# Kernel tuning notes

Hardware: AMD Instinct MI355X
Metric: run time of the kernel (lower is better)

The kernel has to match this reference:

```python
import jax, jax.numpy as jnp
import numpy as np

B, S, D, H, AD, E = 4, 2048, 1024, 2048, 128, 8

def _ln(x, g, b, eps=1e-5):
    m = jnp.mean(x, axis=-1, keepdims=True)
    v = jnp.var(x, axis=-1, keepdims=True)
    return (x - m) * jax.lax.rsqrt(v + eps) * g + b

def setup_inputs() -> dict:
    key = jax.random.key(0)
    ks = jax.random.split(key, 12)
    scale = 1.0 / D ** 0.5
    ascale = scale * 0.01
    ead = 0.01 / AD ** 0.5
    return {
        'x': jax.random.normal(ks[0], (B, S, D), jnp.float32),
        'expert_weights': jax.random.uniform(ks[1], (B, S, E), jnp.float32),
        'Wu': jax.random.normal(ks[2], (H, D), jnp.float32) * scale,
        'bu': jnp.zeros((H,), jnp.float32),
        'Wg': jax.random.normal(ks[3], (H, D), jnp.float32) * scale,
        'bg': jnp.zeros((H,), jnp.float32),
        'Wd': jax.random.normal(ks[4], (D, H), jnp.float32) * scale,
        'bd': jnp.zeros((D,), jnp.float32),
        'Wpre': jax.random.normal(ks[5], (AD, D), jnp.float32) * ascale,
        'bpre': jnp.zeros((AD,), jnp.float32),
        'Wpost': jax.random.normal(ks[6], (AD, H), jnp.float32) * ascale,
        'bpost': jnp.zeros((AD,), jnp.float32),
        'ln_g': jnp.ones((AD,), jnp.float32),
        'ln_b': jnp.zeros((AD,), jnp.float32),
        'Wap': jax.random.normal(ks[7], (H, AD), jnp.float32) * ascale,
        'A': jax.random.normal(ks[8], (E, AD, AD), jnp.float32) * ead,
        'eg': jnp.ones((E, AD), jnp.float32),
        'eb': jnp.zeros((E, AD), jnp.float32),
        'Wp': jax.random.normal(ks[9], (H, AD), jnp.float32) * ead,
        'Wo': jax.random.normal(ks[10], (D, H), jnp.float32) * ead,
    }

def reference(x, expert_weights, Wu, bu, Wg, bg, Wd, bd, Wpre, bpre, Wpost, bpost, ln_g, ln_b, Wap, A, eg, eb, Wp, Wo):
    # ---- SharedExpertMLP ----
    up = x @ Wu.T + bu                      # [B,S,H]
    gate = x @ Wg.T + bg
    hidden = jax.nn.silu(gate) * up
    adapt_in = _ln(x @ Wpre.T + bpre, ln_g, ln_b)        # [B,S,AD]
    adapt_out = _ln(hidden @ Wpost.T + bpost, ln_g, ln_b)
    aw = jnp.einsum('bsa,bta->bst', adapt_in, adapt_out)  # [B,S,S]
    aw = jax.nn.silu(jnp.clip(aw, -5.0, 5.0))
    adapt = jnp.einsum('bst,bta->bsa', aw, adapt_in)
    hidden = hidden + 0.1 * (adapt @ Wap.T)
    shared = hidden @ Wd.T + bd                           # [B,S,D]
    # ---- expert branch (vectorized over experts) ----
    pre = x @ Wpre.T + bpre                               # [B,S,AD] (no adapt_norm here, as in torch)
    h = jnp.einsum('bsa,eca->ebsc', pre, A)               # per-expert adapter linear
    h = _ln(h, eg[:, None, None, :], eb[:, None, None, :])
    wmask = jnp.where(expert_weights > 0, expert_weights, 0.0)  # [B,S,E]
    hw = jnp.einsum('ebsa,bse->bsa', h, wmask)            # weighted combine before shared projections
    Wc = Wo @ Wp                                          # [D,AD]: output_proj(expert_proj(.))
    contrib = hw @ Wc.T                                   # [B,S,D]
    # sum_i w_i * (shared + 0.1*mask_i*expert_i) = shared*sum(w) + 0.1*sum(w_i*expert_i)
    return shared * jnp.sum(expert_weights, axis=-1, keepdims=True) + 0.1 * contrib
```

## Files before the change

kernel.cpp:

```cpp
#include <hip/hip_runtime.h>
#include <math.h>

#define BB 4
#define SS 2048
#define DD 1024
#define HH 2048
#define AD 128
#define EE 8
#define MM (BB*SS)
#define PS 136

typedef unsigned short u16;
typedef short bf16x8 __attribute__((ext_vector_type(8)));
typedef float f32x4 __attribute__((ext_vector_type(4)));
typedef float f32x16 __attribute__((ext_vector_type(16)));

__device__ __forceinline__ float silu_f(float x){ return x / (1.f + __expf(-x)); }

__device__ __forceinline__ u16 f2bf(float f){
    union { float f; unsigned u; } c; c.f = f;
    unsigned r = (c.u + 0x7FFFu + ((c.u >> 16) & 1u)) >> 16;
    return (u16)r;
}

__device__ __forceinline__ void gld16(const u16* g, u16* l){
    __builtin_amdgcn_global_load_lds((const __attribute__((address_space(1))) void*)g,
                                     (__attribute__((address_space(3))) void*)l, 16, 0, 0);
}

#define VMCNT(n) asm volatile("s_waitcnt vmcnt(" #n ")" ::: "memory")

__global__ __launch_bounds__(256,2) void mfma_sk(
    const u16* __restrict__ A, const u16* __restrict__ B, float* __restrict__ P,
    int M, int K, int S, long sA, long sB, long sC, long sSplit)
{
    __shared__ __align__(16) u16 As[128*32];
    __shared__ __align__(16) u16 Bs[128*32];
    const int t = threadIdx.x;
    const int lane = t & 63;
    const int wv = t >> 6;
    const int s = blockIdx.x;
    const int m0 = blockIdx.y * 128;
    const u16* Ab = A + (long)blockIdx.z * sA;
    const u16* Bb = B + (long)blockIdx.z * sB;
    const int srow = t >> 2, scol = (t & 3) * 8;
    const int Ks = K / S, kBeg = s * Ks;
    const u16* ga0 = Ab + (long)(m0 + srow) * K + scol + kBeg;
    const u16* ga1 = ga0 + 64L * K;
    const u16* gb0 = Bb + (long)srow * K + scol + kBeg;
    const u16* gb1 = gb0 + 64L * K;
    u16* la0 = As + t * 8;  u16* la1 = As + 2048 + t * 8;
    u16* lb0 = Bs + t * 8;  u16* lb1 = Bs + 2048 + t * 8;
    const int fr = lane & 15, q = lane >> 4;
    const int wm = (wv & 1) * 64, wn = (wv >> 1) * 64;

    f32x4 acc[4][4] = {};
    for (int k0 = 0; k0 < Ks; k0 += 32) {
        gld16(ga0 + k0, la0);
        gld16(ga1 + k0, la1);
        gld16(gb0 + k0, lb0);
        gld16(gb1 + k0, lb1);
        __syncthreads();
        bf16x8 af[4], bfr[4];
        #pragma unroll
        for (int i = 0; i < 4; ++i) af[i]  = *(const bf16x8*)&As[(wm + i*16 + fr)*32 + q*8];
        #pragma unroll
        for (int i = 0; i < 4; ++i) bfr[i] = *(const bf16x8*)&Bs[(wn + i*16 + fr)*32 + q*8];
        #pragma unroll
        for (int mi = 0; mi < 4; ++mi)
            #pragma unroll
            for (int ni = 0; ni < 4; ++ni)
                acc[mi][ni] = __builtin_amdgcn_mfma_f32_16x16x32_bf16(af[mi], bfr[ni], acc[mi][ni], 0, 0, 0);
        __syncthreads();
    }

    float* Pf = P + (long)s * sSplit + (long)blockIdx.z * sC;
    #pragma unroll
    for (int mi = 0; mi < 4; ++mi)
        #pragma unroll
        for (int ni = 0; ni < 4; ++ni) {
            const int col = wn + ni*16 + fr;
            #pragma unroll
            for (int r = 0; r < 4; ++r) {
                const int row = m0 + wm + mi*16 + q*4 + r;
                Pf[(long)row * 128 + col] = acc[mi][ni][r];
            }
        }
}

__global__ __launch_bounds__(256,2) void mfma_upgate(
    const u16* __restrict__ X, const u16* __restrict__ Wu_, const u16* __restrict__ Wg_,
    const float* __restrict__ bu, const float* __restrict__ bg, u16* __restrict__ H)
{
    __shared__ __align__(16) u16 lds[36864];
    const int t = threadIdx.x, lane = t & 63, wv = t >> 6;
    const int l31 = lane & 31, kh = lane >> 5;
    const int wr = wv & 1, wc = wv >> 1;
    const int m0 = blockIdx.y * 128, n0 = blockIdx.x * 128;

    const int srow = t >> 2;
    const int gcol = (((t & 3) ^ ((t >> 3) & 3)) * 8);
    const u16* gx = X   + (long)(m0 + srow) * DD + gcol;
    const u16* gu = Wu_ + (long)(n0 + srow) * DD + gcol;
    const u16* gg = Wg_ + (long)(n0 + srow) * DD + gcol;
    const int st8 = t * 8;

    const int sw3 = (l31 >> 1) & 3;
    int offA[2][2], offU[2][2], offG[2][2];
    #pragma unroll
    for (int m = 0; m < 2; ++m)
        #pragma unroll
        for (int ks = 0; ks < 2; ++ks) {
            const int ko = ((ks*2 + kh) ^ sw3) * 8;
            offA[m][ks] =        (wr*64 + m*32 + l31)*32 + ko;
            offU[m][ks] = 4096 + (wc*64 + m*32 + l31)*32 + ko;
            offG[m][ks] = 8192 + (wc*64 + m*32 + l31)*32 + ko;
        }

    f32x16 accU[2][2] = {};
    f32x16 accG[2][2] = {};

    auto stage = [&](int tb) {
        u16* Lb = lds + (tb % 3) * 12288;
        const int k0 = tb * 32;
        gld16(gx + k0,           Lb + st8);
        gld16(gx + 64L*DD + k0,  Lb + 2048 + st8);
        gld16(gu + k0,           Lb + 4096 + st8);
        gld16(gu + 64L*DD + k0,  Lb + 6144 + st8);
        gld16(gg + k0,           Lb + 8192 + st8);
        gld16(gg + 64L*DD + k0,  Lb + 10240 + st8);
    };

    auto compute = [&](int tb) {
        const u16* Lb = lds + (tb % 3) * 12288;
        bf16x8 a[2][2], uf[2][2], gf[2][2];
        #pragma unroll
        for (int n = 0; n < 2; ++n)
            #pragma unroll
            for (int ks = 0; ks < 2; ++ks) {
                uf[n][ks] = *(const bf16x8*)&Lb[offU[n][ks]];
                gf[n][ks] = *(const bf16x8*)&Lb[offG[n][ks]];
            }
        #pragma unroll
        for (int m = 0; m < 2; ++m)
            #pragma unroll
            for (int ks = 0; ks < 2; ++ks)
                a[m][ks] = *(const bf16x8*)&Lb[offA[m][ks]];
        __builtin_amdgcn_s_setprio(1);
        #pragma unroll
        for (int m = 0; m < 2; ++m)
            #pragma unroll
            for (int n = 0; n < 2; ++n)
                #pragma unroll
                for (int ks = 0; ks < 2; ++ks) {
                    accU[m][n] = __builtin_amdgcn_mfma_f32_32x32x16_bf16(a[m][ks], uf[n][ks], accU[m][n], 0, 0, 0);
                    accG[m][n] = __builtin_amdgcn_mfma_f32_32x32x16_bf16(a[m][ks], gf[n][ks], accG[m][n], 0, 0, 0);
                }
        __builtin_amdgcn_s_setprio(0);
    };

    stage(0); stage(1);
    #pragma unroll 1
    for (int tt = 0; tt < 30; ++tt) {
        VMCNT(6);
        __builtin_amdgcn_s_barrier();
        __builtin_amdgcn_sched_barrier(0);
        stage(tt + 2);
        compute(tt);
    }
    VMCNT(6);
    __builtin_amdgcn_s_barrier();
    __builtin_amdgcn_sched_barrier(0);
    compute(30);
    VMCNT(0);
    __builtin_amdgcn_s_barrier();
    __builtin_amdgcn_sched_barrier(0);
    compute(31);

    #pragma unroll
    for (int n = 0; n < 2; ++n) {
        const int col = n0 + wc*64 + n*32 + l31;
        const float bub = bu[col], bgb = bg[col];
        #pragma unroll
        for (int m = 0; m < 2; ++m)
            #pragma unroll
            for (int r = 0; r < 16; ++r) {
                const int row = m0 + wr*64 + m*32 + (r & 3) + 8*(r >> 2) + 4*kh;
                const float u = accU[m][n][r] + bub;
                const float g = accG[m][n][r] + bgb;
                H[(long)row * HH + col] = f2bf(silu_f(g) * u);
            }
    }
}

__global__ __launch_bounds__(256,2) void mfma_final(
    const u16* __restrict__ Hh, const u16* __restrict__ Wd_,
    const u16* __restrict__ Ac, const u16* __restrict__ Wcat,
    const float* __restrict__ bd, const float* __restrict__ sumw,
    float* __restrict__ out)
{
    __shared__ __align__(16) u16 lds[24576];
    const int t = threadIdx.x, lane = t & 63, wv = t >> 6;
    const int l31 = lane & 31, kh = lane >> 5;
    const int wr = wv & 1, wc = wv >> 1;
    const int m0 = blockIdx.y * 128, n0 = blockIdx.x * 128;

    const int srow = t >> 2;
    const int gcol = (((t & 3) ^ ((t >> 3) & 3)) * 8);
    const u16* gA1 = Hh   + (long)(m0 + srow) * HH  + gcol;
    const u16* gB1 = Wd_  + (long)(n0 + srow) * HH  + gcol;
    const u16* gA2 = Ac   + (long)(m0 + srow) * 256 + gcol;
    const u16* gB2 = Wcat + (long)(n0 + srow) * 256 + gcol;
    const int st8 = t * 8;

    const int sw3 = (l31 >> 1) & 3;
    int offA[2][2], offB[2][2];
    #pragma unroll
    for (int m = 0; m < 2; ++m)
        #pragma unroll
        for (int ks = 0; ks < 2; ++ks) {
            const int ko = ((ks*2 + kh) ^ sw3) * 8;
            offA[m][ks] =        (wr*64 + m*32 + l31)*32 + ko;
            offB[m][ks] = 4096 + (wc*64 + m*32 + l31)*32 + ko;
        }

    f32x16 acc[2][2]  = {};
    f32x16 acc2[2][2] = {};

    auto stage = [&](int tk) {
        u16* Lb = lds + (tk % 3) * 8192;
        if (tk < 64) {
            const int k0 = tk * 32;
            gld16(gA1 + k0,           Lb + st8);
            gld16(gA1 + 64L*HH + k0,  Lb + 2048 + st8);
            gld16(gB1 + k0,           Lb + 4096 + st8);
            gld16(gB1 + 64L*HH + k0,  Lb + 6144 + st8);
        } else {
            const int k0 = (tk - 64) * 32;
            gld16(gA2 + k0,           Lb + st8);
            gld16(gA2 + 64L*256 + k0, Lb + 2048 + st8);
            gld16(gB2 + k0,           Lb + 4096 + st8);
            gld16(gB2 + 64L*256 + k0, Lb + 6144 + st8);
        }
    };

    auto compute = [&](int tk, f32x16 (&A)[2][2]) {
        const u16* Lb = lds + (tk % 3) * 8192;
        bf16x8 a[2][2], b[2][2];
        #pragma unroll
        for (int m = 0; m < 2; ++m)
            #pragma unroll
            for (int ks = 0; ks < 2; ++ks) {
                a[m][ks] = *(const bf16x8*)&Lb[offA[m][ks]];
                b[m][ks] = *(const bf16x8*)&Lb[offB[m][ks]];
            }
        __builtin_amdgcn_s_setprio(1);
        #pragma unroll
        for (int m = 0; m < 2; ++m)
            #pragma unroll
            for (int n = 0; n < 2; ++n)
                #pragma unroll
                for (int ks = 0; ks < 2; ++ks)
                    A[m][n] = __builtin_amdgcn_mfma_f32_32x32x16_bf16(a[m][ks], b[n][ks], A[m][n], 0, 0, 0);
        __builtin_amdgcn_s_setprio(0);
    };

    stage(0); stage(1);
    #pragma unroll 1
    for (int tt = 0; tt < 70; ++tt) {
        VMCNT(4);
        __builtin_amdgcn_s_barrier();
        __builtin_amdgcn_sched_barrier(0);
        stage(tt + 2);
        if (tt < 64) compute(tt, acc); else compute(tt, acc2);
    }
    VMCNT(4);
    __builtin_amdgcn_s_barrier();
    __builtin_amdgcn_sched_barrier(0);
    compute(70, acc2);
    VMCNT(0);
    __builtin_amdgcn_s_barrier();
    __builtin_amdgcn_sched_barrier(0);
    compute(71, acc2);

    #pragma unroll
    for (int n = 0; n < 2; ++n) {
        const int col = n0 + wc*64 + n*32 + l31;
        const float bdc = bd[col];
        #pragma unroll
        for (int m = 0; m < 2; ++m)
            #pragma unroll
            for (int r = 0; r < 16; ++r) {
                const int row = m0 + wr*64 + m*32 + (r & 3) + 8*(r >> 2) + 4*kh;
                out[(long)row * DD + col] =
                    sumw[row] * (acc[m][n][r] + bdc) + 0.1f * acc2[m][n][r];
            }
    }
}

__global__ __launch_bounds__(256,2) void flash_pv(
    const u16* __restrict__ ai, const u16* __restrict__ ao,
    const u16* __restrict__ aiT, float* __restrict__ adaptP)
{
    __shared__ __align__(16) u16 As[128*32];
    __shared__ __align__(16) u16 Bs[128*32];
    __shared__ __align__(16) u16 Psh[128*PS];
    const int t = threadIdx.x, lane = t & 63, wv = t >> 6;
    const int fr = lane & 15, q = lane >> 4;
    const int wm = (wv & 1) * 64, wn = (wv >> 1) * 64;
    const int tg = blockIdx.x, s0 = blockIdx.y * 128, b = blockIdx.z;
    const u16* aib  = ai  + (long)b * SS * AD;
    const u16* aob  = ao  + (long)b * SS * AD;
    const u16* aiTb = aiT + (long)b * AD * SS;
    const int srow = t >> 2, scol = (t & 3) * 8;
    u16* la0 = As + t * 8;  u16* la1 = As + 2048 + t * 8;
    u16* lb0 = Bs + t * 8;  u16* lb1 = Bs + 2048 + t * 8;
    const u16* ga0 = aib + (long)(s0 + srow) * AD + scol;
    const u16* ga1 = ga0 + 64L * AD;

    f32x4 vacc[4][4] = {};
    for (int ti = 0; ti < 2; ++ti) {
        const int t0 = tg * 256 + ti * 128;
        const u16* gb0 = aob + (long)(t0 + srow) * AD + scol;
        const u16* gb1 = gb0 + 64L * AD;
        f32x4 acc[4][4] = {};
        for (int k0 = 0; k0 < AD; k0 += 32) {
            gld16(ga0 + k0, la0);
            gld16(ga1 + k0, la1);
            gld16(gb0 + k0, lb0);
            gld16(gb1 + k0, lb1);
            __syncthreads();
            bf16x8 af[4], bfr[4];
            #pragma unroll
            for (int i = 0; i < 4; ++i) af[i]  = *(const bf16x8*)&As[(wm + i*16 + fr)*32 + q*8];
            #pragma unroll
            for (int i = 0; i < 4; ++i) bfr[i] = *(const bf16x8*)&Bs[(wn + i*16 + fr)*32 + q*8];
            #pragma unroll
            for (int mi = 0; mi < 4; ++mi)
                #pragma unroll
                for (int ni = 0; ni < 4; ++ni)
                    acc[mi][ni] = __builtin_amdgcn_mfma_f32_16x16x32_bf16(af[mi], bfr[ni], acc[mi][ni], 0, 0, 0);
            __syncthreads();
        }
        #pragma unroll
        for (int mi = 0; mi < 4; ++mi)
            #pragma unroll
            for (int ni = 0; ni < 4; ++ni)
                #pragma unroll
                for (int r = 0; r < 4; ++r) {
                    float v = acc[mi][ni][r];
                    v = fminf(fmaxf(v, -5.f), 5.f);
                    Psh[(wm + mi*16 + q*4 + r)*PS + wn + ni*16 + fr] = f2bf(silu_f(v));
                }
        __syncthreads();
        #pragma unroll
        for (int kk = 0; kk < 4; ++kk) {
            bf16x8 pf[4], bi[4];
            #pragma unroll
            for (int mi = 0; mi < 4; ++mi)
                pf[mi] = *(const bf16x8*)&Psh[(wm + mi*16 + fr)*PS + kk*32 + q*8];
            #pragma unroll
            for (int ni = 0; ni < 4; ++ni)
                bi[ni] = *(const bf16x8*)&aiTb[(long)(wn + ni*16 + fr)*SS + t0 + kk*32 + q*8];
            #pragma unroll
            for (int mi = 0; mi < 4; ++mi)
                #pragma unroll
                for (int ni = 0; ni < 4; ++ni)
                    vacc[mi][ni] = __builtin_amdgcn_mfma_f32_16x16x32_bf16(pf[mi], bi[ni], vacc[mi][ni], 0, 0, 0);
        }
    }
    float* Pf = adaptP + (long)tg * MM * AD + (long)(b * SS + s0) * AD;
    #pragma unroll
    for (int mi = 0; mi < 4; ++mi)
        #pragma unroll
        for (int ni = 0; ni < 4; ++ni) {
            const int col = wn + ni*16 + fr;
            #pragma unroll
            for (int r = 0; r < 4; ++r) {
                const int row = wm + mi*16 + q*4 + r;
                Pf[(long)row * AD + col] = vacc[mi][ni][r];
            }
        }
}

__global__ __launch_bounds__(256) void scale_adapt(
    const float* __restrict__ P, const float* __restrict__ sumw, u16* __restrict__ acat)
{
    const int i = blockIdx.x * 256 + threadIdx.x;
    float4 v = ((const float4*)P)[i];
    #pragma unroll
    for (int tg = 1; tg < 8; ++tg) {
        const float4 w = ((const float4*)P)[i + (long)tg * (MM*AD/4)];
        v.x += w.x; v.y += w.y; v.z += w.z; v.w += w.w;
    }
    const long grow = i >> 5;
    const float sw = sumw[grow];
    ushort4 o;
    o.x = f2bf(sw*v.x); o.y = f2bf(sw*v.y); o.z = f2bf(sw*v.z); o.w = f2bf(sw*v.w);
    ((ushort4*)acat)[grow*64 + 32 + (i & 31)] = o;
}

__global__ __launch_bounds__(256) void expert_fused(
    const u16* __restrict__ pre, const u16* __restrict__ aexp,
    const float* __restrict__ ew, const float* __restrict__ eg,
    const float* __restrict__ eb, u16* __restrict__ acat,
    float* __restrict__ sumw)
{
    __shared__ float ewsh[32*8];
    __shared__ float egsh[8*128], ebsh[8*128];
    __shared__ float part[32*132];
    const int t = threadIdx.x, lane = t & 63, wv = t >> 6;
    const int fr = lane & 15, q = lane >> 4;
    const int wm = (wv & 1) * 16;
    const int e0 = (wv >> 1) * 4;
    const int m0 = blockIdx.x * 32;
    if (t < 64) {
        const int row = t >> 1, j = (t & 1)*4;
        *(float4*)&ewsh[row*8+j] = *(const float4*)&ew[(long)(m0+row)*EE + j];
    }
    {   const int e = t >> 5, c = (t & 31)*4;
        *(float4*)&egsh[e*128+c] = *(const float4*)&eg[e*128+c];
        *(float4*)&ebsh[e*128+c] = *(const float4*)&eb[e*128+c]; }
    __syncthreads();

    f32x4 hwacc[8] = {};
    for (int ee = 0; ee < 4; ++ee) {
        const int e = e0 + ee;
        f32x4 acc[8] = {};
        const u16* Ae = aexp + (long)e * AD * AD;
        #pragma unroll
        for (int ks = 0; ks < 4; ++ks) {
            bf16x8 af, bfr[8];
            af = *(const bf16x8*)&pre[(long)(m0 + wm + fr)*AD + ks*32 + q*8];
            #pragma unroll
            for (int ni = 0; ni < 8; ++ni)
                bfr[ni] = *(const bf16x8*)&Ae[(long)(ni*16 + fr)*AD + ks*32 + q*8];
            #pragma unroll
            for (int ni = 0; ni < 8; ++ni)
                acc[ni] = __builtin_amdgcn_mfma_f32_16x16x32_bf16(af, bfr[ni], acc[ni], 0, 0, 0);
        }
        #pragma unroll
        for (int r = 0; r < 4; ++r) {
            float s = 0.f, s2 = 0.f;
            #pragma unroll
            for (int ni = 0; ni < 8; ++ni) { const float v = acc[ni][r]; s += v; s2 += v*v; }
            #pragma unroll
            for (int msk = 1; msk < 16; msk <<= 1) {
                s  += __shfl_xor(s,  msk, 64);
                s2 += __shfl_xor(s2, msk, 64);
            }
            const float mean = s * (1.f/128.f);
            const float var  = s2 * (1.f/128.f) - mean*mean;
            const float rs   = rsqrtf(var + 1e-5f);
            const int rowl = wm + q*4 + r;
            float w = ewsh[rowl*8 + e]; w = w > 0.f ? w : 0.f;
            #pragma unroll
            for (int ni = 0; ni < 8; ++ni) {
                const int col = ni*16 + fr;
                hwacc[ni][r] += w * ((acc[ni][r] - mean) * rs * egsh[e*128+col] + ebsh[e*128+col]);
            }
        }
    }
    if (wv >= 2) {
        #pragma unroll
        for (int r = 0; r < 4; ++r) {
            const int rowl = wm + q*4 + r;
            #pragma unroll
            for (int ni = 0; ni < 8; ++ni)
                part[rowl*132 + ni*16 + fr] = hwacc[ni][r];
        }
    }
    __syncthreads();
    if (wv < 2) {
        #pragma unroll
        for (int r = 0; r < 4; ++r) {
            const int rowl = wm + q*4 + r;
            #pragma unroll
            for (int ni = 0; ni < 8; ++ni) {
                const float v = hwacc[ni][r] + part[rowl*132 + ni*16 + fr];
                acat[(long)(m0+rowl)*256 + ni*16 + fr] = f2bf(v);
            }
            if (fr == 0) {
                float sw = 0.f;
                #pragma unroll
                for (int j = 0; j < 8; ++j) sw += ewsh[rowl*8 + j];
                sumw[m0 + rowl] = sw;
            }
        }
    }
}

template<int S>
__global__ __launch_bounds__(128) void ln_reduce(
    const float* __restrict__ P, long sSplit, const float* __restrict__ bias,
    u16* __restrict__ raw, u16* __restrict__ ln_out,
    const float* __restrict__ g, const float* __restrict__ b)
{
    const int r = blockIdx.x, tid = threadIdx.x;
    float v = bias[tid];
    #pragma unroll
    for (int s = 0; s < S; ++s) v += P[(long)s * sSplit + (long)r * AD + tid];
    if (raw) raw[(long)r * AD + tid] = f2bf(v);
    __shared__ float red[AD], red2[AD];
    red[tid] = v; red2[tid] = v*v;
    __syncthreads();
    for (int s = 64; s > 0; s >>= 1) {
        if (tid < s) { red[tid] += red[tid+s]; red2[tid] += red2[tid+s]; }
        __syncthreads();
    }
    const float mean = red[0] * (1.f/AD);
    const float var  = red2[0] * (1.f/AD) - mean*mean;
    const float rs   = rsqrtf(var + 1e-5f);
    ln_out[(long)r * AD + tid] = f2bf((v - mean) * rs * g[tid] + b[tid]);
}

__global__ __launch_bounds__(256) void reduce_cat(
    const float* __restrict__ P, u16* __restrict__ Wcat)
{
    const int i = blockIdx.x * 256 + threadIdx.x;
    const int a4 = i & 31, z = (i >> 5) & 1, d = i >> 6;
    const float* src = P + (long)z * (16L*DD*AD) + (long)d * AD + a4*4;
    float4 v = *(const float4*)src;
    #pragma unroll
    for (int s = 1; s < 16; ++s) {
        const float4 w = *(const float4*)(src + (long)s * DD * AD);
        v.x += w.x; v.y += w.y; v.z += w.z; v.w += w.w;
    }
    ushort4 o; o.x=f2bf(v.x); o.y=f2bf(v.y); o.z=f2bf(v.z); o.w=f2bf(v.w);
    ((ushort4*)Wcat)[(long)d*64 + z*32 + a4] = o;
}

__global__ __launch_bounds__(256) void transpose6(
    const u16* __restrict__ wRaw, u16* __restrict__ wT,
    const u16* __restrict__ ai, u16* __restrict__ aiT)
{
    __shared__ u16 tile[32][33];
    const int z = blockIdx.z;
    const u16* in; u16* out;
    if (z < 2) { in = wRaw + (long)z * HH * AD; out = wT + (long)z * AD * HH; }
    else       { in = ai + (long)(z-2) * SS * AD; out = aiT + (long)(z-2) * AD * SS; }
    const int x0 = blockIdx.x * 32, y0 = blockIdx.y * 32;
    const int tx = threadIdx.x & 31, ty = threadIdx.x >> 5;
    #pragma unroll
    for (int j = 0; j < 4; ++j)
        tile[ty + j*8][tx] = in[(long)(y0 + ty + j*8) * AD + x0 + tx];
    __syncthreads();
    #pragma unroll
    for (int j = 0; j < 4; ++j)
        out[(long)(x0 + ty + j*8) * SS + y0 + tx] = tile[tx][ty + j*8];
}

struct Cvt5 { const float* in[5]; u16* out[5]; long cum[6]; };
__global__ __launch_bounds__(256) void cvt_pack(Cvt5 a)
{
    const long i = (long)blockIdx.x * 256 + threadIdx.x;
    if (i >= a.cum[5]) return;
    int s = 0;
    while (i >= a.cum[s+1]) ++s;
    const long j = i - a.cum[s];
    const float4 v = ((const float4*)a.in[s])[j];
    ushort4 o;
    o.x = f2bf(v.x); o.y = f2bf(v.y); o.z = f2bf(v.z); o.w = f2bf(v.w);
    ((ushort4*)a.out[s])[j] = o;
}

extern "C" void kernel_launch(void* const* d_in, const int* in_sizes, int n_in,
                              void* d_out, int out_size, void* d_ws, size_t ws_size,
                              hipStream_t stream) {
    const float* x    = (const float*)d_in[0];
    const float* ew   = (const float*)d_in[1];
    const float* Wu   = (const float*)d_in[2];
    const float* bu   = (const float*)d_in[3];
    const float* Wg   = (const float*)d_in[4];
    const float* bg   = (const float*)d_in[5];
    const float* Wd   = (const float*)d_in[6];
    const float* bd   = (const float*)d_in[7];
    const float* Wpre = (const float*)d_in[8];
    const float* bpre = (const float*)d_in[9];
    const float* Wpost= (const float*)d_in[10];
    const float* bpost= (const float*)d_in[11];
    const float* ln_g = (const float*)d_in[12];
    const float* ln_b = (const float*)d_in[13];
    const float* Wap  = (const float*)d_in[14];
    const float* Aex  = (const float*)d_in[15];
    const float* eg   = (const float*)d_in[16];
    const float* eb   = (const float*)d_in[17];
    const float* Wp   = (const float*)d_in[18];
    const float* Wo   = (const float*)d_in[19];
    float* out = (float*)d_out;

    char* p = (char*)d_ws;
    auto take = [&](long bytes) -> char* {
        char* r = p; p += (bytes + 255) & ~255L; return r;
    };
    u16* x_slot  = (u16*)take(16777216);
    u16* wslot   = (u16*)take((long)2*DD*HH*2);
    u16* wpre    = (u16*)take((long)AD*DD*2);
    u16* aex     = (u16*)take((long)EE*AD*AD*2);
    u16* pre_bf  = (u16*)take((long)MM*AD*2);
    u16* ai_bf   = (u16*)take((long)MM*AD*2);
    char* shareA = take(33554432);
    u16* acat    = (u16*)take((long)MM*256*2);
    float* sumw  = (float*)take((long)MM*4);
    u16* hidden  = (u16*)take((long)MM*HH*2);

    u16* x_bf    = x_slot;
    u16* aiT     = x_slot;
    u16* wRaw    = aiT  + 1048576;
    u16* wT      = wRaw + 524288;
    u16* wpost_w = wT   + 524288;
    u16* wcat    = wpost_w + 262144;
    u16* ao_bf   = wcat + 262144;
    float* preP   = (float*)shareA;
    float* wcP    = (float*)(shareA + 16777216);
    float* wpostP = (float*)shareA;
    float* adaptP = (float*)shareA;

    {
        Cvt5 a;
        a.in[0]=x;    a.out[0]=x_bf;              long n0=(long)MM*DD/4;
        a.in[1]=Wu;   a.out[1]=wslot;             long n1=(long)HH*DD/4;
        a.in[2]=Wg;   a.out[2]=wslot+(long)DD*HH; long n2=(long)HH*DD/4;
        a.in[3]=Wpre; a.out[3]=wpre;              long n3=(long)AD*DD/4;
        a.in[4]=Aex;  a.out[4]=aex;               long n4=(long)EE*AD*AD/4;
        a.cum[0]=0; a.cum[1]=n0; a.cum[2]=n0+n1; a.cum[3]=n0+n1+n2;
        a.cum[4]=n0+n1+n2+n3; a.cum[5]=n0+n1+n2+n3+n4;
        cvt_pack<<<dim3((a.cum[5]+255)/256), 256, 0, stream>>>(a);
    }
    mfma_sk<<<dim3(4, MM/128, 1), 256, 0, stream>>>(
        x_bf, wpre, preP, MM, DD, 4, 0, 0, 0, (long)MM*AD);
    ln_reduce<4><<<dim3(MM), 128, 0, stream>>>(preP, (long)MM*AD, bpre, pre_bf, ai_bf, ln_g, ln_b);
    expert_fused<<<dim3(MM/32), 256, 0, stream>>>(pre_bf, aex, ew, eg, eb, acat, sumw);
    mfma_upgate<<<dim3(HH/128, MM/128), 256, 0, stream>>>(
        x_bf, wslot, wslot+(long)DD*HH, bu, bg, hidden);
    {
        Cvt5 a;
        a.in[0]=Wo;    a.out[0]=wslot;             long n0=(long)DD*HH/4;
        a.in[1]=Wd;    a.out[1]=wslot+(long)DD*HH; long n1=(long)DD*HH/4;
        a.in[2]=Wpost; a.out[2]=wpost_w;           long n2=(long)AD*HH/4;
        a.in[3]=Wp;    a.out[3]=wRaw;              long n3=(long)HH*AD/4;
        a.in[4]=Wap;   a.out[4]=wRaw+(long)HH*AD;  long n4=(long)HH*AD/4;
        a.cum[0]=0; a.cum[1]=n0; a.cum[2]=n0+n1; a.cum[3]=n0+n1+n2;
        a.cum[4]=n0+n1+n2+n3; a.cum[5]=n0+n1+n2+n3+n4;
        cvt_pack<<<dim3((a.cum[5]+255)/256), 256, 0, stream>>>(a);
    }
    transpose6<<<dim3(4,64,6), 256, 0, stream>>>(wRaw, wT, ai_bf, aiT);
    mfma_sk<<<dim3(16, DD/128, 2), 256, 0, stream>>>(
        wslot, wT, wcP, DD, HH, 16, (long)DD*HH, (long)AD*HH, 16L*DD*AD, (long)DD*AD);
    reduce_cat<<<dim3(256), 256, 0, stream>>>(wcP, wcat);
    mfma_sk<<<dim3(8, MM/128, 1), 256, 0, stream>>>(
        hidden, wpost_w, wpostP, MM, HH, 8, 0, 0, 0, (long)MM*AD);
    ln_reduce<8><<<dim3(MM), 128, 0, stream>>>(wpostP, (long)MM*AD, bpost, nullptr, ao_bf, ln_g, ln_b);
    flash_pv<<<dim3(8, SS/128, BB), 256, 0, stream>>>(ai_bf, ao_bf, aiT, adaptP);
    scale_adapt<<<dim3((long)MM*AD/4/256), 256, 0, stream>>>(adaptP, sumw, acat);
    mfma_final<<<dim3(DD/128, MM/128), 256, 0, stream>>>(
        hidden, wslot+(long)DD*HH, acat, wcat, bd, sumw, out);
}
```

Before: 398.4 us.

## Enlarge upgate GEMM tile to 256x128 with 512 threads and 4-stage pipeline

Restructures the fused up/gate GEMM kernel to use 512-thread blocks, each covering 256 rows by 128 columns. Each wave now computes a 128x32 tile, and the LDS pipeline deepens from 3 to 4 stages using 128KB of shared memory. The larger tile is meant to cut redundant weight loads from global memory per output and to hide more load latency. The cost is higher LDS usage, which may limit occupancy to one block per CU, plus a changed register footprint per thread.

```diff
diff --git a/kernel.cpp b/kernel.cpp
--- a/kernel.cpp
+++ b/kernel.cpp
@@ -88,87 +88,86 @@
         }
 }
 
-__global__ __launch_bounds__(256,2) void mfma_upgate(
+__global__ __launch_bounds__(512,2) void mfma_upgate(
     const u16* __restrict__ X, const u16* __restrict__ Wu_, const u16* __restrict__ Wg_,
     const float* __restrict__ bu, const float* __restrict__ bg, u16* __restrict__ H)
 {
-    __shared__ __align__(16) u16 lds[36864];
+    __shared__ __align__(16) u16 lds[65536];
     const int t = threadIdx.x, lane = t & 63, wv = t >> 6;
     const int l31 = lane & 31, kh = lane >> 5;
-    const int wr = wv & 1, wc = wv >> 1;
-    const int m0 = blockIdx.y * 128, n0 = blockIdx.x * 128;
+    const int wr = wv >> 2, wc = wv & 3;
+    const int m0 = blockIdx.y * 256, n0 = blockIdx.x * 128;
 
     const int srow = t >> 2;
     const int gcol = (((t & 3) ^ ((t >> 3) & 3)) * 8);
-    const u16* gx = X   + (long)(m0 + srow) * DD + gcol;
-    const u16* gu = Wu_ + (long)(n0 + srow) * DD + gcol;
-    const u16* gg = Wg_ + (long)(n0 + srow) * DD + gcol;
+    const u16* gx0 = X   + (long)(m0 + srow) * DD + gcol;
+    const u16* gx1 = gx0 + 128L * DD;
+    const u16* gu  = Wu_ + (long)(n0 + srow) * DD + gcol;
+    const u16* gg  = Wg_ + (long)(n0 + srow) * DD + gcol;
     const int st8 = t * 8;
 
     const int sw3 = (l31 >> 1) & 3;
-    int offA[2][2], offU[2][2], offG[2][2];
-    #pragma unroll
-    for (int m = 0; m < 2; ++m)
+    int offA[4][2], offB[2];
+    #pragma unroll
+    for (int m = 0; m < 4; ++m)
+        #pragma unroll
+        for (int ks = 0; ks < 2; ++ks)
+            offA[m][ks] = (wr*128 + m*32 + l31)*32 + (((ks*2 + kh) ^ sw3) * 8);
+    #pragma unroll
+    for (int ks = 0; ks < 2; ++ks)
+        offB[ks] = (wc*32 + l31)*32 + (((ks*2 + kh) ^ sw3) * 8);
+
+    f32x16 accU[4] = {};
+    f32x16 accG[4] = {};
+
+    auto stage = [&](int tb) {
+        u16* Lb = lds + (tb & 3) * 16384;
+        const int k0 = tb * 32;
+        gld16(gx0 + k0, Lb + st8);
+        gld16(gx1 + k0, Lb + 4096 + st8);
+        gld16(gu  + k0, Lb + 8192 + st8);
+        gld16(gg  + k0, Lb + 12288 + st8);
+    };
+
+    auto compute = [&](int tb) {
+        const u16* Lb = lds + (tb & 3) * 16384;
+        bf16x8 a[4][2], uf[2], gf[2];
         #pragma unroll
         for (int ks = 0; ks < 2; ++ks) {
-            const int ko = ((ks*2 + kh) ^ sw3) * 8;
-            offA[m][ks] =        (wr*64 + m*32 + l31)*32 + ko;
-            offU[m][ks] = 4096 + (wc*64 + m*32 + l31)*32 + ko;
-            offG[m][ks] = 8192 + (wc*64 + m*32 + l31)*32 + ko;
-        }
-
-    f32x16 accU[2][2] = {};
-    f32x16 accG[2][2] = {};
-
-    auto stage = [&](int tb) {
-        u16* Lb = lds + (tb % 3) * 12288;
-        const int k0 = tb * 32;
-        gld16(gx + k0,           Lb + st8);
-        gld16(gx + 64L*DD + k0,  Lb + 2048 + st8);
-        gld16(gu + k0,           Lb + 4096 + st8);
-        gld16(gu + 64L*DD + k0,  Lb + 6144 + st8);
-        gld16(gg + k0,           Lb + 8192 + st8);
-        gld16(gg + 64L*DD + k0,  Lb + 10240 + st8);
-    };
-
-    auto compute = [&](int tb) {
-        const u16* Lb = lds + (tb % 3) * 12288;
-        bf16x8 a[2][2], uf[2][2], gf[2][2];
-        #pragma unroll
-        for (int n = 0; n < 2; ++n)
-            #pragma unroll
-            for (int ks = 0; ks < 2; ++ks) {
-                uf[n][ks] = *(const bf16x8*)&Lb[offU[n][ks]];
-                gf[n][ks] = *(const bf16x8*)&Lb[offG[n][ks]];
-            }
-        #pragma unroll
-        for (int m = 0; m < 2; ++m)
+            uf[ks] = *(const bf16x8*)&Lb[8192  + offB[ks]];
+            gf[ks] = *(const bf16x8*)&Lb[12288 + offB[ks]];
+        }
+        #pragma unroll
+        for (int m = 0; m < 4; ++m)
             #pragma unroll
             for (int ks = 0; ks < 2; ++ks)
                 a[m][ks] = *(const bf16x8*)&Lb[offA[m][ks]];
         __builtin_amdgcn_s_setprio(1);
         #pragma unroll
-        for (int m = 0; m < 2; ++m)
-            #pragma unroll
-            for (int n = 0; n < 2; ++n)
-                #pragma unroll
-                for (int ks = 0; ks < 2; ++ks) {
-                    accU[m][n] = __builtin_amdgcn_mfma_f32_32x32x16_bf16(a[m][ks], uf[n][ks], accU[m][n], 0, 0, 0);
-                    accG[m][n] = __builtin_amdgcn_mfma_f32_32x32x16_bf16(a[m][ks], gf[n][ks], accG[m][n], 0, 0, 0);
-                }
+        for (int m = 0; m < 4; ++m)
+            #pragma unroll
+            for (int ks = 0; ks < 2; ++ks) {
+                accU[m] = __builtin_amdgcn_mfma_f32_32x32x16_bf16(a[m][ks], uf[ks], accU[m], 0, 0, 0);
+                accG[m] = __builtin_amdgcn_mfma_f32_32x32x16_bf16(a[m][ks], gf[ks], accG[m], 0, 0, 0);
+            }
         __builtin_amdgcn_s_setprio(0);
     };
 
-    stage(0); stage(1);
+    stage(0); stage(1); stage(2);
+
     #pragma unroll 1
-    for (int tt = 0; tt < 30; ++tt) {
-        VMCNT(6);
+    for (int tt = 0; tt < 29; ++tt) {
+        VMCNT(8);
         __builtin_amdgcn_s_barrier();
         __builtin_amdgcn_sched_barrier(0);
-        stage(tt + 2);
+        stage(tt + 3);
         compute(tt);
     }
-    VMCNT(6);
+    VMCNT(8);
+    __builtin_amdgcn_s_barrier();
+    __builtin_amdgcn_sched_barrier(0);
+    compute(29);
+    VMCNT(4);
     __builtin_amdgcn_s_barrier();
     __builtin_amdgcn_sched_barrier(0);
     compute(30);
@@ -177,20 +176,18 @@
     __builtin_amdgcn_sched_barrier(0);
     compute(31);
 
-    #pragma unroll
-    for (int n = 0; n < 2; ++n) {
-        const int col = n0 + wc*64 + n*32 + l31;
-        const float bub = bu[col], bgb = bg[col];
-        #pragma unroll
-        for (int m = 0; m < 2; ++m)
-            #pragma unroll
-            for (int r = 0; r < 16; ++r) {
-                const int row = m0 + wr*64 + m*32 + (r & 3) + 8*(r >> 2) + 4*kh;
-                const float u = accU[m][n][r] + bub;
-                const float g = accG[m][n][r] + bgb;
-                H[(long)row * HH + col] = f2bf(silu_f(g) * u);
-            }
-    }
+    const int col = n0 + wc*32 + l31;
+    const float bub = bu[col], bgb = bg[col];
+    u16* Hp = H + (long)(m0 + wr*128) * HH + col;
+    #pragma unroll
+    for (int m = 0; m < 4; ++m)
+        #pragma unroll
+        for (int r = 0; r < 16; ++r) {
+            const int rowl = m*32 + (r & 3) + 8*(r >> 2) + 4*kh;
+            const float u = accU[m][r] + bub;
+            const float g = accG[m][r] + bgb;
+            Hp[(long)rowl * HH] = f2bf(silu_f(g) * u);
+        }
 }
 
 __global__ __launch_bounds__(256,2) void mfma_final(
@@ -631,7 +628,7 @@
         x_bf, wpre, preP, MM, DD, 4, 0, 0, 0, (long)MM*AD);
     ln_reduce<4><<<dim3(MM), 128, 0, stream>>>(preP, (long)MM*AD, bpre, pre_bf, ai_bf, ln_g, ln_b);
     expert_fused<<<dim3(MM/32), 256, 0, stream>>>(pre_bf, aex, ew, eg, eb, acat, sumw);
-    mfma_upgate<<<dim3(HH/128, MM/128), 256, 0, stream>>>(
+    mfma_upgate<<<dim3(HH/128, MM/256), 512, 0, stream>>>(
         x_bf, wslot, wslot+(long)DD*HH, bu, bg, hidden);
     {
         Cvt5 a;
```

Result: no change. 399.3 us (+0.2%).
